# Performance work log

Measured on AMD Instinct MI355X. Metric: run time of the kernel, lower is better.

Reference implementation:

```python
import jax, jax.numpy as jnp
import numpy as np

B, S, CTX, DIM = 2, 2048, 2048, 2048
H, HKV, HD = 16, 4, 128
HID = 5464  # 4*ceil(int(4*DIM*2/3)/4)
EPS = 1.1920929e-07  # torch eps=None -> finfo(fp32).eps
REP = H // HKV


def rmsnorm(x, w):
    return x * jax.lax.rsqrt(jnp.mean(x * x, axis=-1, keepdims=True) + EPS) * w


def rotate_half(x):
    # interleaved rotate: out[::2] = -x[1::2], out[1::2] = x[::2]
    x2 = x.reshape(x.shape[:-1] + (-1, 2))
    return jnp.stack([-x2[..., 1], x2[..., 0]], axis=-1).reshape(x.shape)


def masked_attn(q, k, v, mask):
    # q,k,v: [B,H,Sq/Sk,D]; mask broadcastable to [B,H,Sq,Sk]
    scale = 1.0 / jnp.sqrt(jnp.asarray(q.shape[-1], q.dtype))
    s = jnp.einsum('bhqd,bhkd->bhqk', q, k) * scale
    s = jnp.where(mask, s, jnp.asarray(-1e30, s.dtype))
    p = jax.nn.softmax(s, axis=-1)
    p = jnp.where(mask, p, 0.0)  # fully-masked rows -> 0 output (flex_attention semantics)
    return jnp.einsum('bhqk,bhkd->bhqd', p, v)


def setup_inputs() -> dict:
    key = jax.random.key(0)
    ks = jax.random.split(key, 20)
    std = 0.02
    return {
        'x': jax.random.normal(ks[0], (B, S, DIM), jnp.float32),
        'context': jax.random.normal(ks[1], (B, CTX, DIM), jnp.float32),
        'freqs_cos': jax.random.uniform(ks[2], (S, 1, HD), jnp.float32),
        'freqs_sin': jax.random.uniform(ks[3], (S, 1, HD), jnp.float32),
        'wqkv': jax.random.normal(ks[4], ((H + 2 * HKV) * HD, DIM), jnp.float32) * std,
        'wo_self': jax.random.normal(ks[5], (DIM, DIM), jnp.float32) * std,
        'qn_self': jnp.ones((HD,), jnp.float32),
        'kn_self': jnp.ones((HD,), jnp.float32),
        'wq': jax.random.normal(ks[6], (H * HD, DIM), jnp.float32) * std,
        'wkv': jax.random.normal(ks[7], (2 * HKV * HD, DIM), jnp.float32) * std,
        'wo_cross': jax.random.normal(ks[8], (DIM, DIM), jnp.float32) * std,
        'qn_cross': jnp.ones((HD,), jnp.float32),
        'kn_cross': jnp.ones((HD,), jnp.float32),
        'w1': jax.random.normal(ks[9], (HID, DIM), jnp.float32) * std,
        'w2': jax.random.normal(ks[10], (DIM, HID), jnp.float32) * std,
        'attn_norm_w': jnp.ones((DIM,), jnp.float32),
        'cross_norm_w': jnp.ones((DIM,), jnp.float32),
        'ffn_norm_w': jnp.ones((DIM,), jnp.float32),
        'vis_mask': jax.random.randint(ks[11], (B, S), 0, 2).astype(bool),
        'context_mask': jax.random.randint(ks[12], (B, CTX), 0, 2).astype(bool),
    }


def reference(x, context, freqs_cos, freqs_sin, wqkv, wo_self, qn_self, kn_self,
              wq, wkv, wo_cross, qn_cross, kn_cross, w1, w2,
              attn_norm_w, cross_norm_w, ffn_norm_w, vis_mask, context_mask):
    b, s, _ = x.shape
    ctx = context.shape[1]

    # ---- self-attention (prenorm) ----
    h0 = rmsnorm(x, attn_norm_w)
    qkv = h0 @ wqkv.T
    xq = qkv[..., :H * HD].reshape(b, s, H, HD)
    xk = qkv[..., H * HD:(H + HKV) * HD].reshape(b, s, HKV, HD)
    xv = qkv[..., (H + HKV) * HD:].reshape(b, s, HKV, HD)
    xq = rmsnorm(xq, qn_self)   # qk-norm BEFORE rope in self-attn
    xk = rmsnorm(xk, kn_self)
    xq = xq * freqs_cos + rotate_half(xq) * freqs_sin
    xk = xk * freqs_cos + rotate_half(xk) * freqs_sin
    q = xq.transpose(0, 2, 1, 3)
    k = jnp.repeat(xk.transpose(0, 2, 1, 3), REP, axis=1)
    v = jnp.repeat(xv.transpose(0, 2, 1, 3), REP, axis=1)
    m_self = vis_mask[:, None, :, None] & vis_mask[:, None, None, :]
    a = masked_attn(q, k, v, m_self)
    h = x + a.transpose(0, 2, 1, 3).reshape(b, s, DIM) @ wo_self.T

    # ---- cross-attention (prenorm) ----
    hc = rmsnorm(h, cross_norm_w)
    xq = (hc @ wq.T).reshape(b, s, H, HD)
    kv = context @ wkv.T
    xk = kv[..., :HKV * HD].reshape(b, ctx, HKV, HD)
    xv = kv[..., HKV * HD:].reshape(b, ctx, HKV, HD)
    xq = xq * freqs_cos + rotate_half(xq) * freqs_sin  # rope on q BEFORE qk-norm in cross-attn
    xq = rmsnorm(xq, qn_cross)
    xk = rmsnorm(xk, kn_cross)
    q = xq.transpose(0, 2, 1, 3)
    k = jnp.repeat(xk.transpose(0, 2, 1, 3), REP, axis=1)
    v = jnp.repeat(xv.transpose(0, 2, 1, 3), REP, axis=1)
    m_cross = context_mask[:, None, None, :]
    a = masked_attn(q, k, v, m_cross)
    h = h + a.transpose(0, 2, 1, 3).reshape(b, s, DIM) @ wo_cross.T

    # ---- FFN (silu) ----
    hf = rmsnorm(h, ffn_norm_w)
    return h + jax.nn.silu(hf @ w1.T) @ w2.T
```

## Files before the change

### kernel.cpp

```cpp
#include <hip/hip_runtime.h>

#define DEVI __device__ __forceinline__

typedef __attribute__((ext_vector_type(4))) float f32x4;
typedef __attribute__((ext_vector_type(8))) __bf16 bf16x8;

static constexpr float EPS = 1.1920929e-07f;
static constexpr float SC2L = 0.12751551960234575f;

DEVI float bf2f(unsigned short u){ return __uint_as_float(((unsigned)u)<<16); }
DEVI unsigned short f2bfu(float f){
  unsigned u = __float_as_uint(f);
  u += 0x7fffu + ((u>>16)&1u);
  return (unsigned short)(u>>16);
}
DEVI unsigned pack2(float a, float b){ return (unsigned)f2bfu(a) | ((unsigned)f2bfu(b)<<16); }
DEVI float exp2a(float x){ float r; asm("v_exp_f32 %0, %1" : "=v"(r) : "v"(x)); return r; }
DEVI unsigned cvtpk(float lo, float hi){
  unsigned r; asm("v_cvt_pk_bf16_f32 %0, %1, %2" : "=v"(r) : "v"(lo), "v"(hi)); return r;
}

DEVI void gload16(const void* g, const void* l){
  __builtin_amdgcn_global_load_lds((const __attribute__((address_space(1))) void*)g,
                                   (__attribute__((address_space(3))) void*)l, 16, 0, 0);
}

__global__ void k_masknorm(const unsigned* __restrict__ vin, const unsigned* __restrict__ cin,
                           unsigned char* __restrict__ vout, unsigned char* __restrict__ cout){
  __shared__ int smode;
  const int t = threadIdx.x;
  if (t==0) smode = 0;
  __syncthreads();
  unsigned loc = 0;
  for (int i=t; i<1024; i+=256) loc |= (vin[i] > 1u);
  if (loc) smode = 1;
  __syncthreads();
  if (smode){
    for (int i=t; i<1024; i+=256){
      ((unsigned*)vout)[i] = vin[i];
      ((unsigned*)cout)[i] = cin[i];
    }
  } else {
    const int* vi = (const int*)vin; const int* ci = (const int*)cin;
    for (int i=t; i<4096; i+=256){
      vout[i] = (unsigned char)(vi[i] != 0);
      cout[i] = (unsigned char)(ci[i] != 0);
    }
  }
}

__global__ void k_conv(const float* __restrict__ s, unsigned short* __restrict__ d, int n4){
  int i = blockIdx.x*256 + threadIdx.x;
  if (i >= n4) return;
  float4 v = ((const float4*)s)[i];
  uint2 u; u.x = pack2(v.x, v.y); u.y = pack2(v.z, v.w);
  ((uint2*)d)[i] = u;
}
__global__ void k_convpad_rows(const float* __restrict__ s, unsigned short* __restrict__ d,
                               int R, int C, int Rp){
  int i = blockIdx.x*256 + threadIdx.x;
  int total = (Rp*C)>>2;
  if (i >= total) return;
  uint2 u; u.x = 0u; u.y = 0u;
  if (i*4 < R*C){ float4 v = ((const float4*)s)[i]; u.x = pack2(v.x,v.y); u.y = pack2(v.z,v.w); }
  ((uint2*)d)[i] = u;
}
__global__ void k_convpad_cols(const float* __restrict__ s, unsigned short* __restrict__ d,
                               int N, int K, int Kp){
  int i = blockIdx.x*256 + threadIdx.x;
  int total = (N*Kp)>>2;
  if (i >= total) return;
  int i4 = i*4; int n = i4/Kp; int k = i4 - n*Kp;
  uint2 u; u.x = 0u; u.y = 0u;
  if (k < K){ float4 v = *(const float4*)(s + (size_t)n*K + k); u.x = pack2(v.x,v.y); u.y = pack2(v.z,v.w); }
  ((uint2*)d)[i] = u;
}

__global__ void k_rms(const float* __restrict__ X, const float* __restrict__ W,
                      unsigned short* __restrict__ Y){
  const int row = blockIdx.x, tid = threadIdx.x;
  const float* x = X + (size_t)row*2048;
  float4 v0 = ((const float4*)x)[tid*2];
  float4 v1 = ((const float4*)x)[tid*2+1];
  float ss = v0.x*v0.x+v0.y*v0.y+v0.z*v0.z+v0.w*v0.w
           + v1.x*v1.x+v1.y*v1.y+v1.z*v1.z+v1.w*v1.w;
  #pragma unroll
  for (int o=32;o;o>>=1) ss += __shfl_xor(ss, o);
  __shared__ float red[4];
  if ((tid&63)==0) red[tid>>6] = ss;
  __syncthreads();
  float tot = red[0]+red[1]+red[2]+red[3];
  float rs = rsqrtf(tot*(1.0f/2048.0f) + EPS);
  float4 w0 = ((const float4*)W)[tid*2];
  float4 w1 = ((const float4*)W)[tid*2+1];
  uint4 u;
  u.x = pack2(v0.x*rs*w0.x, v0.y*rs*w0.y);
  u.y = pack2(v0.z*rs*w0.z, v0.w*rs*w0.w);
  u.z = pack2(v1.x*rs*w1.x, v1.y*rs*w1.y);
  u.w = pack2(v1.z*rs*w1.z, v1.w*rs*w1.w);
  *(uint4*)(Y + (size_t)row*2048 + tid*8) = u;
}

template<int EPI>
__global__ void k_gemm(const unsigned short* __restrict__ A, const unsigned short* __restrict__ Bw,
                       void* Cout, const float* resid, int M, int N, int K){
  __shared__ __align__(16) unsigned short sm[16384];
  const int tid = threadIdx.x;
  const int w = tid>>6, l = tid&63, g = l>>4, q = l&15;
  const int bm = blockIdx.y<<7, bn = blockIdx.x<<7;
  const int wr = (w>>1)<<6, wc = (w&1)<<6;
  f32x4 acc[4][4];
  #pragma unroll
  for (int a=0;a<4;++a)
    #pragma unroll
    for (int b2=0;b2<4;++b2) acc[a][b2] = f32x4{0.f,0.f,0.f,0.f};

  const unsigned short* Ag = A + (size_t)bm*K;
  const unsigned short* Bg = Bw + (size_t)bn*K;
  const int nk = K>>5;
  int cur = 0;

  auto STAGE = [&](int buf, int kt){
    #pragma unroll
    for (int i=0;i<2;++i){
      int L = (i*256+tid)*16;
      int r = L>>6; int ce = (L&63)>>1;
      int lofs = __builtin_amdgcn_readfirstlane(buf*8192 + i*4096 + (tid>>6)*1024);
      gload16(Ag + (size_t)r*K + (kt<<5) + ce, (const char*)sm + lofs);
    }
    #pragma unroll
    for (int i=0;i<2;++i){
      int L = (i*256+tid)*16;
      int r = L>>6; int ce = (L&63)>>1;
      int lofs = __builtin_amdgcn_readfirstlane(16384 + buf*8192 + i*4096 + (tid>>6)*1024);
      gload16(Bg + (size_t)r*K + (kt<<5) + ce, (const char*)sm + lofs);
    }
  };

  STAGE(0, 0);
  __syncthreads();
  for (int kt=0; kt<nk; ++kt){
    if (kt+1 < nk) STAGE(cur^1, kt+1);
    const unsigned short* Ab = sm + cur*4096;
    const unsigned short* Bb = sm + 8192 + cur*4096;
    bf16x8 af[4], bfr[4];
    #pragma unroll
    for (int mi=0;mi<4;++mi) af[mi] = *(const bf16x8*)(Ab + (wr + mi*16 + q)*32 + g*8);
    #pragma unroll
    for (int ni=0;ni<4;++ni) bfr[ni] = *(const bf16x8*)(Bb + (wc + ni*16 + q)*32 + g*8);
    #pragma unroll
    for (int mi=0;mi<4;++mi)
      #pragma unroll
      for (int ni=0;ni<4;++ni)
        acc[mi][ni] = __builtin_amdgcn_mfma_f32_16x16x32_bf16(af[mi], bfr[ni], acc[mi][ni], 0,0,0);
    __syncthreads();
    cur ^= 1;
  }
  #pragma unroll
  for (int mi=0;mi<4;++mi)
    #pragma unroll
    for (int ni=0;ni<4;++ni)
      #pragma unroll
      for (int r=0;r<4;++r){
        int row = bm + wr + mi*16 + g*4 + r;
        int col = bn + wc + ni*16 + q;
        size_t idx = (size_t)row*N + col;
        float v = acc[mi][ni][r];
        if (EPI==0) ((unsigned short*)Cout)[idx] = f2bfu(v);
        else if (EPI==1){ float sg = v/(1.0f+__expf(-v)); ((unsigned short*)Cout)[idx] = f2bfu(sg); }
        else ((float*)Cout)[idx] = resid[idx] + v;
      }
}

template<int EPI>
__global__ __launch_bounds__(512,1)
void k_gemm2(const unsigned short* __restrict__ A, const unsigned short* __restrict__ Bw,
             void* Cout, const float* resid, int M, int N, int K){
  __shared__ __align__(16) char sm[147456];
  const int tid = threadIdx.x;
  const int wid = tid>>6, l = tid&63, g = l>>4, q = l&15;
  const int wm = wid>>2, wn = wid&3;
  const int gy = gridDim.y;
  const int orig = blockIdx.y*gridDim.x + blockIdx.x;
  const int qq = (gridDim.x*gy)>>3;
  const int nid = (orig&7)*qq + (orig>>3);
  const int bm = (nid % gy) << 7;
  const int bn = (nid / gy) << 8;
  f32x4 acc[4][4];
  #pragma unroll
  for (int a=0;a<4;++a)
    #pragma unroll
    for (int b2=0;b2<4;++b2) acc[a][b2] = f32x4{0.f,0.f,0.f,0.f};

  const unsigned short* Ag = A + (size_t)bm*K;
  const unsigned short* Bg = Bw + (size_t)bn*K;
  const int nk = K>>6;

  auto STAGE_A = [&](int buf, int kt){
    #pragma unroll
    for (int j=0;j<2;++j){
      int L = (j*512+tid)*16;
      int lr = L>>7, c8 = (L>>4)&7;
      int cg = c8 ^ (lr&7);
      int lofs = __builtin_amdgcn_readfirstlane(buf*49152 + j*8192 + wid*1024);
      gload16(Ag + (size_t)lr*K + (kt<<6) + cg*8, sm + lofs);
    }
  };
  auto STAGE_B1 = [&](int buf, int kt, int j){
    int L = (j*512+tid)*16;
    int rn = L>>7, c8 = (L>>4)&7;
    int cg = c8 ^ (rn&7);
    int lofs = __builtin_amdgcn_readfirstlane(buf*49152 + 16384 + j*8192 + wid*1024);
    gload16(Bg + (size_t)rn*K + (kt<<6) + cg*8, sm + lofs);
  };

  STAGE_A(0,0); STAGE_B1(0,0,0); STAGE_B1(0,0,1); STAGE_B1(0,0,2); STAGE_B1(0,0,3);
  STAGE_A(1,1); STAGE_B1(1,1,0); STAGE_B1(1,1,1); STAGE_B1(1,1,2); STAGE_B1(1,1,3);

  int buf = 0;
  for (int kt=0; kt<nk; ++kt){
    int p2 = buf+2; if (p2>2) p2-=3;
    if (kt+1 < nk) asm volatile("s_waitcnt vmcnt(6)" ::: "memory");
    else           asm volatile("s_waitcnt vmcnt(0)" ::: "memory");
    asm volatile("s_waitcnt lgkmcnt(0)" ::: "memory");
    __builtin_amdgcn_s_barrier();
    asm volatile("" ::: "memory");

    const char* Ab = sm + buf*49152;
    const char* Bb = sm + buf*49152 + 16384;

    #pragma unroll
    for (int ks=0; ks<2; ++ks){
      if (kt+2 < nk){
        if (ks==0){ STAGE_A(p2, kt+2); STAGE_B1(p2, kt+2, 0); }
        else      { STAGE_B1(p2, kt+2, 1); STAGE_B1(p2, kt+2, 2); STAGE_B1(p2, kt+2, 3); }
      }
      bf16x8 af[4], bfr[4];
      #pragma unroll
      for (int mi=0;mi<4;++mi){
        int lr = wm*64 + mi*16 + q;
        af[mi] = *(const bf16x8*)(Ab + lr*128 + (((ks*4+g) ^ (lr&7))<<4));
      }
      #pragma unroll
      for (int ni=0;ni<4;++ni){
        int rn = wn*64 + ni*16 + q;
        bfr[ni] = *(const bf16x8*)(Bb + rn*128 + (((ks*4+g) ^ (rn&7))<<4));
      }
      asm volatile("s_waitcnt lgkmcnt(0)" ::: "memory");
      __builtin_amdgcn_s_setprio(1);
      #pragma unroll
      for (int mi=0;mi<4;++mi)
        #pragma unroll
        for (int ni=0;ni<4;++ni)
          acc[mi][ni] = __builtin_amdgcn_mfma_f32_16x16x32_bf16(af[mi], bfr[ni], acc[mi][ni], 0,0,0);
      __builtin_amdgcn_s_setprio(0);
    }
    buf = (buf==2) ? 0 : buf+1;
  }

  #pragma unroll
  for (int mi=0;mi<4;++mi)
    #pragma unroll
    for (int ni=0;ni<4;++ni)
      #pragma unroll
      for (int r=0;r<4;++r){
        int row = bm + wm*64 + mi*16 + g*4 + r;
        int col = bn + wn*64 + ni*16 + q;
        size_t idx = (size_t)row*N + col;
        float v = acc[mi][ni][r];
        if (EPI==0) ((unsigned short*)Cout)[idx] = f2bfu(v);
        else if (EPI==1){ float sg = v/(1.0f+__expf(-v)); ((unsigned short*)Cout)[idx] = f2bfu(sg); }
        else ((float*)Cout)[idx] = resid[idx] + v;
      }
}

__global__ void k_self_pp(const unsigned short* __restrict__ qkv, const float* __restrict__ fc,
                          const float* __restrict__ fs, const float* __restrict__ qn,
                          const float* __restrict__ kn,
                          unsigned short* __restrict__ Qb, unsigned short* __restrict__ Kb,
                          unsigned short* __restrict__ Vt){
  const int row = blockIdx.x;
  const int b = row>>11, s = row&2047;
  const int w = threadIdx.x>>6, l = threadIdx.x&63;
  const int d0 = 2*l, d1 = d0+1;
  const float c0 = fc[s*128+d0], c1 = fc[s*128+d1];
  const float s0 = fs[s*128+d0], s1 = fs[s*128+d1];
  #pragma unroll
  for (int it=0; it<6; ++it){
    const int hh = it*4 + w;
    const unsigned short* src = qkv + (size_t)row*3072 + hh*128;
    if (hh >= 20){
      const int hv = hh - 20;
      size_t base = ((size_t)(b*4 + hv))*128*2048;
      Vt[base + (size_t)d0*2048 + s] = src[d0];
      Vt[base + (size_t)d1*2048 + s] = src[d1];
    } else {
      float x0 = bf2f(src[d0]), x1 = bf2f(src[d1]);
      float ss = x0*x0 + x1*x1;
      #pragma unroll
      for (int o=32;o;o>>=1) ss += __shfl_xor(ss, o);
      float rs = rsqrtf(ss*(1.0f/128.0f) + EPS);
      if (hh < 16){
        float y0 = x0*rs*qn[d0], y1 = x1*rs*qn[d1];
        *(unsigned*)(Qb + (((size_t)(b*16 + hh)*2048 + s)*128) + d0)
          = pack2((y0*c0 - y1*s0)*SC2L, (y1*c1 + y0*s1)*SC2L);
      } else {
        float y0 = x0*rs*kn[d0], y1 = x1*rs*kn[d1];
        *(unsigned*)(Kb + (((size_t)(b*4 + (hh-16))*2048 + s)*128) + d0)
          = pack2(y0*c0 - y1*s0, y1*c1 + y0*s1);
      }
    }
  }
}

__global__ void k_crossq_pp(const unsigned short* __restrict__ qc, const float* __restrict__ fc,
                            const float* __restrict__ fs, const float* __restrict__ qn,
                            unsigned short* __restrict__ Qb){
  const int row = blockIdx.x;
  const int b = row>>11, s = row&2047;
  const int w = threadIdx.x>>6, l = threadIdx.x&63;
  const int d0 = 2*l, d1 = d0+1;
  const float c0 = fc[s*128+d0], c1 = fc[s*128+d1];
  const float s0 = fs[s*128+d0], s1 = fs[s*128+d1];
  #pragma unroll
  for (int it=0; it<4; ++it){
    const int hh = it*4 + w;
    const unsigned short* src = qc + (size_t)row*2048 + hh*128;
    float x0 = bf2f(src[d0]), x1 = bf2f(src[d1]);
    float y0 = x0*c0 - x1*s0;
    float y1 = x1*c1 + x0*s1;
    float ss = y0*y0 + y1*y1;
    #pragma unroll
    for (int o=32;o;o>>=1) ss += __shfl_xor(ss, o);
    float rs = rsqrtf(ss*(1.0f/128.0f) + EPS);
    *(unsigned*)(Qb + (((size_t)(b*16 + hh)*2048 + s)*128) + d0)
      = pack2(y0*rs*qn[d0]*SC2L, y1*rs*qn[d1]*SC2L);
  }
}

__global__ void k_crosskv_pp(const unsigned short* __restrict__ kvc, const float* __restrict__ kn,
                             unsigned short* __restrict__ Kb, unsigned short* __restrict__ Vt){
  const int row = blockIdx.x;
  const int b = row>>11, s = row&2047;
  const int w = threadIdx.x>>6, l = threadIdx.x&63;
  const int d0 = 2*l, d1 = d0+1;
  #pragma unroll
  for (int it=0; it<2; ++it){
    const int hh = it*4 + w;
    const unsigned short* src = kvc + (size_t)row*1024 + hh*128;
    if (hh < 4){
      float x0 = bf2f(src[d0]), x1 = bf2f(src[d1]);
      float ss = x0*x0 + x1*x1;
      #pragma unroll
      for (int o=32;o;o>>=1) ss += __shfl_xor(ss, o);
      float rs = rsqrtf(ss*(1.0f/128.0f) + EPS);
      *(unsigned*)(Kb + (((size_t)(b*4 + hh)*2048 + s)*128) + d0)
        = pack2(x0*rs*kn[d0], x1*rs*kn[d1]);
    } else {
      const int hv = hh-4;
      size_t base = ((size_t)(b*4 + hv))*128*2048;
      Vt[base + (size_t)d0*2048 + s] = src[d0];
      Vt[base + (size_t)d1*2048 + s] = src[d1];
    }
  }
}

template<bool QMASK>
__global__ __launch_bounds__(1024,1)
void k_attn(const unsigned short* __restrict__ Qg, const unsigned short* __restrict__ Kg,
            const unsigned short* __restrict__ Vtg,
            const unsigned char* __restrict__ qm, const unsigned char* __restrict__ km,
            unsigned short* __restrict__ Og, int H, int HKV){
  constexpr int SK = 2048, SQ = 2048, NT = SK/64;
  __shared__ __align__(16) char smem[106496];
  const int qt = blockIdx.x, hk = blockIdx.y, b = blockIdx.z;
  const int REP = H/HKV;
  const int tid = threadIdx.x, w = tid>>6, l = tid&63, g = l>>4, q = l&15;
  const int hq = w>>2, wsub = w&3;

  if (tid < 256){
    const unsigned long long mv = ((const unsigned long long*)(km + (size_t)b*SK))[tid];
    float* bl = (float*)(smem + 98304);
    #pragma unroll
    for (int j=0;j<8;++j)
      bl[tid*8+j] = ((mv>>(8*j)) & 0xffull) ? 0.0f : -3.0e38f;
  }

  const int h = hk*REP + hq;
  const size_t qrow = (size_t)(b*H + h)*SQ + qt*64 + wsub*16 + q;
  bf16x8 qf[4];
  #pragma unroll
  for (int ks=0;ks<4;++ks) qf[ks] = *(const bf16x8*)(Qg + qrow*128 + ks*32 + g*8);

  f32x4 oacc[8];
  #pragma unroll
  for (int i=0;i<8;++i) oacc[i] = f32x4{0.f,0.f,0.f,0.f};
  float m_run = -1.0e30f, l_run = 0.f;

  const unsigned short* Kt0 = Kg + (size_t)(b*HKV + hk)*SK*128;
  const unsigned short* Vt0 = Vtg + (size_t)(b*HKV + hk)*128*SK;
  const float* biasf = (const float*)(smem + 98304);
  char* Pl = smem + 65536 + w*2048;

  auto STAGE_T = [&](int t, int p){
    {
      int r = tid>>4, c16 = tid&15;
      int c = (c16 & 8) | ((c16 & 7) ^ (r & 7));
      int lofs = __builtin_amdgcn_readfirstlane(p*16384 + w*1024);
      gload16(Kt0 + (size_t)(t*64 + r)*128 + c*8, smem + lofs);
    }
    {
      int d = tid>>3, c8 = tid&7;
      int c = c8 ^ (d & 7);
      int lofs = __builtin_amdgcn_readfirstlane(32768 + p*16384 + w*1024);
      gload16(Vt0 + (size_t)d*SK + t*64 + c*8, smem + lofs);
    }
  };

  STAGE_T(0, 0);

  for (int t=0; t<NT; ++t){
    const int p = t&1;
    asm volatile("s_waitcnt lgkmcnt(0)" ::: "memory");
    __builtin_amdgcn_s_barrier();
    asm volatile("" ::: "memory");
    if (t+1 < NT){
      STAGE_T(t+1, p^1);
      asm volatile("s_waitcnt vmcnt(2)" ::: "memory");
    } else {
      asm volatile("s_waitcnt vmcnt(0)" ::: "memory");
    }
    __builtin_amdgcn_s_barrier();
    asm volatile("" ::: "memory");

    const char* Kb_ = smem + p*16384;
    const char* Vb_ = smem + 32768 + p*16384;

    f32x4 sacc[4];
    #pragma unroll
    for (int i=0;i<4;++i) sacc[i] = f32x4{0.f,0.f,0.f,0.f};
    __builtin_amdgcn_s_setprio(1);
    #pragma unroll
    for (int ks=0;ks<4;++ks){
      #pragma unroll
      for (int mi=0;mi<4;++mi){
        int kcol = mi*16 + q;
        int c = 4*ks + g;
        int c16 = (c & 8) | ((c & 7) ^ (kcol & 7));
        bf16x8 ak = *(const bf16x8*)(Kb_ + kcol*256 + c16*16);
        sacc[mi] = __builtin_amdgcn_mfma_f32_16x16x32_bf16(ak, qf[ks], sacc[mi], 0,0,0);
      }
    }
    __builtin_amdgcn_s_setprio(0);

    float sv[4][4];
    float mloc = -3.0e38f;
    #pragma unroll
    for (int mi=0;mi<4;++mi){
      f32x4 bb = *(const f32x4*)(biasf + t*64 + mi*16 + g*4);
      #pragma unroll
      for (int r=0;r<4;++r){
        float v = sacc[mi][r] + bb[r];
        sv[mi][r] = v;
        mloc = fmaxf(mloc, v);
      }
    }
    mloc = fmaxf(mloc, __shfl_xor(mloc, 16));
    mloc = fmaxf(mloc, __shfl_xor(mloc, 32));
    if (!__all(mloc - m_run <= 8.0f)){
      float mnew = fmaxf(m_run, mloc);
      float alpha = exp2a(m_run - mnew);
      l_run *= alpha;
      #pragma unroll
      for (int i=0;i<8;++i) oacc[i] *= alpha;
      m_run = mnew;
    }
    float rsum = 0.f;
    unsigned pb[4][2];
    #pragma unroll
    for (int mi=0;mi<4;++mi){
      float p0 = exp2a(sv[mi][0] - m_run);
      float p1 = exp2a(sv[mi][1] - m_run);
      float p2 = exp2a(sv[mi][2] - m_run);
      float p3 = exp2a(sv[mi][3] - m_run);
      rsum += (p0+p1)+(p2+p3);
      pb[mi][0] = cvtpk(p0, p1);
      pb[mi][1] = cvtpk(p2, p3);
    }
    rsum += __shfl_xor(rsum, 16);
    rsum += __shfl_xor(rsum, 32);
    l_run += rsum;

    #pragma unroll
    for (int mi=0;mi<4;++mi){
      int c16 = (2*mi + (g>>1)) ^ (q & 7);
      uint2 uu; uu.x = pb[mi][0]; uu.y = pb[mi][1];
      *(uint2*)(Pl + q*128 + c16*16 + (g&1)*8) = uu;
    }
    asm volatile("" ::: "memory");

    __builtin_amdgcn_s_setprio(1);
    #pragma unroll
    for (int ks=0;ks<2;++ks){
      int c16 = (4*ks + g) ^ (q & 7);
      bf16x8 pf = *(const bf16x8*)(Pl + q*128 + c16*16);
      #pragma unroll
      for (int mi=0;mi<8;++mi){
        int d = mi*16 + q;
        bf16x8 vf = *(const bf16x8*)(Vb_ + d*128 + c16*16);
        oacc[mi] = __builtin_amdgcn_mfma_f32_16x16x32_bf16(vf, pf, oacc[mi], 0,0,0);
      }
    }
    __builtin_amdgcn_s_setprio(0);
  }

  float inv = (l_run > 0.f) ? 1.0f/l_run : 0.f;
  if (QMASK){
    if (!qm[(size_t)b*SQ + qt*64 + wsub*16 + q]) inv = 0.f;
  }
  float* Ot = (float*)smem;
  const int qloc = tid>>4, seg = tid&15;
  #pragma unroll
  for (int ph=0; ph<4; ++ph){
    __syncthreads();
    if (hq == ph){
      #pragma unroll
      for (int mi=0;mi<8;++mi)
        #pragma unroll
        for (int r=0;r<4;++r){
          int d = mi*16 + g*4 + r;
          Ot[d*65 + wsub*16 + q] = oacc[mi][r]*inv;
        }
    }
    __syncthreads();
    int srow = qt*64 + qloc;
    size_t obase = ((size_t)b*SQ + srow)*(size_t)(H*128) + (size_t)(hk*REP + ph)*128 + seg*8;
    float vv[8];
    #pragma unroll
    for (int j=0;j<8;++j) vv[j] = Ot[(seg*8 + j)*65 + qloc];
    uint4 u;
    u.x = pack2(vv[0],vv[1]); u.y = pack2(vv[2],vv[3]);
    u.z = pack2(vv[4],vv[5]); u.w = pack2(vv[6],vv[7]);
    *(uint4*)(Og + obase) = u;
  }
}

extern "C" void kernel_launch(void* const* d_in, const int* in_sizes, int n_in,
                              void* d_out, int out_size, void* d_ws, size_t ws_size,
                              hipStream_t stream){
  const float* x        = (const float*)d_in[0];
  const float* ctx      = (const float*)d_in[1];
  const float* fc       = (const float*)d_in[2];
  const float* fs       = (const float*)d_in[3];
  const float* wqkv     = (const float*)d_in[4];
  const float* wo_self  = (const float*)d_in[5];
  const float* qn_self  = (const float*)d_in[6];
  const float* kn_self  = (const float*)d_in[7];
  const float* wq       = (const float*)d_in[8];
  const float* wkv      = (const float*)d_in[9];
  const float* wo_cross = (const float*)d_in[10];
  const float* qn_cross = (const float*)d_in[11];
  const float* kn_cross = (const float*)d_in[12];
  const float* w1       = (const float*)d_in[13];
  const float* w2       = (const float*)d_in[14];
  const float* attn_nw  = (const float*)d_in[15];
  const float* cross_nw = (const float*)d_in[16];
  const float* ffn_nw   = (const float*)d_in[17];
  const unsigned* vis_raw   = (const unsigned*)d_in[18];
  const unsigned* cmask_raw = (const unsigned*)d_in[19];
  float* out = (float*)d_out;

  char* ws = (char*)d_ws;
  unsigned short* wslot = (unsigned short*)(ws);
  unsigned short* ctxbf = (unsigned short*)(ws +  23068672);
  unsigned short* nbuf  = (unsigned short*)(ws +  39845888);
  unsigned short* qkvb  = (unsigned short*)(ws +  56623104);
  unsigned short* Qb    = (unsigned short*)(ws +  81788928);
  unsigned short* Kb    = (unsigned short*)(ws +  98566144);
  unsigned short* Vtb   = (unsigned short*)(ws + 102760448);
  unsigned short* aob   = (unsigned short*)(ws + 106954752);
  unsigned short* midb  = (unsigned short*)(ws + 106954752);
  unsigned char*  visN  = (unsigned char*)(ws + 153092096);
  unsigned char*  cmkN  = (unsigned char*)(ws + 153096192);
  unsigned short* qcb   = qkvb;
  unsigned short* kvcb  = qkvb + 8388608;

  auto conv = [&](const float* s, unsigned short* dst, size_t n){
    int n4 = (int)(n>>2);
    k_conv<<<(n4+255)/256, 256, 0, stream>>>(s, dst, n4);
  };

  k_masknorm<<<1,256,0,stream>>>(vis_raw, cmask_raw, visN, cmkN);

  conv(ctx, ctxbf, (size_t)4096*2048);
  k_rms<<<4096,256,0,stream>>>(x, attn_nw, nbuf);
  conv(wqkv, wslot, (size_t)3072*2048);
  k_gemm2<0><<<dim3(12,32),512,0,stream>>>(nbuf, wslot, qkvb, nullptr, 4096,3072,2048);
  k_self_pp<<<4096,256,0,stream>>>(qkvb, fc, fs, qn_self, kn_self, Qb, Kb, Vtb);
  k_attn<true><<<dim3(32,4,2),1024,0,stream>>>(Qb, Kb, Vtb, visN, visN, aob, 16, 4);
  conv(wo_self, wslot, (size_t)2048*2048);
  k_gemm2<2><<<dim3(8,32),512,0,stream>>>(aob, wslot, out, x, 4096,2048,2048);

  k_rms<<<4096,256,0,stream>>>(out, cross_nw, nbuf);
  conv(wq, wslot, (size_t)2048*2048);
  k_gemm2<0><<<dim3(8,32),512,0,stream>>>(nbuf, wslot, qcb, nullptr, 4096,2048,2048);
  conv(wkv, wslot, (size_t)1024*2048);
  k_gemm<0><<<dim3(8,32),256,0,stream>>>(ctxbf, wslot, kvcb, nullptr, 4096,1024,2048);
  k_crossq_pp<<<4096,256,0,stream>>>(qcb, fc, fs, qn_cross, Qb);
  k_crosskv_pp<<<4096,256,0,stream>>>(kvcb, kn_cross, Kb, Vtb);
  k_attn<false><<<dim3(32,4,2),1024,0,stream>>>(Qb, Kb, Vtb, nullptr, cmkN, aob, 16, 4);
  conv(wo_cross, wslot, (size_t)2048*2048);
  k_gemm2<2><<<dim3(8,32),512,0,stream>>>(aob, wslot, out, out, 4096,2048,2048);

  k_rms<<<4096,256,0,stream>>>(out, ffn_nw, nbuf);
  k_convpad_rows<<<(5632*2048/4+255)/256,256,0,stream>>>(w1, wslot, 5464, 2048, 5632);
  k_gemm2<1><<<dim3(22,32),512,0,stream>>>(nbuf, wslot, midb, nullptr, 4096,5632,2048);
  k_convpad_cols<<<(2048*5632/4+255)/256,256,0,stream>>>(w2, wslot, 2048, 5464, 5632);
  k_gemm2<2><<<dim3(8,32),512,0,stream>>>(midb, wslot, out, out, 4096,2048,5632);

  (void)in_sizes; (void)n_in; (void)out_size; (void)ws_size;
}
```

Baseline: 765.2 us.

## Halve GEMM K-tile to 32 to cut LDS and allow multiple blocks per CU

Shrinks the k_gemm2 K step from 64 to 32, so the triple-buffered LDS footprint drops from 144KB to 72KB. The launch bound is raised to allow up to 4 blocks per CU, and the swizzle and staging are rewritten for 64-byte rows. Prefetch is now issued once per iteration ahead of the fragment loads, with a sched_barrier added. The goal is more resident waves to hide memory latency, at the cost of twice as many barriers and a shorter MFMA run per synchronization. A register cap from the new launch bound could cause spills.

```diff
diff --git a/kernel.cpp b/kernel.cpp
--- a/kernel.cpp
+++ b/kernel.cpp
@@ -173,10 +173,10 @@
 }
 
 template<int EPI>
-__global__ __launch_bounds__(512,1)
+__global__ __launch_bounds__(512,4)
 void k_gemm2(const unsigned short* __restrict__ A, const unsigned short* __restrict__ Bw,
              void* Cout, const float* resid, int M, int N, int K){
-  __shared__ __align__(16) char sm[147456];
+  __shared__ __align__(16) char sm[73728];
   const int tid = threadIdx.x;
   const int wid = tid>>6, l = tid&63, g = l>>4, q = l&15;
   const int wm = wid>>2, wn = wid&3;
@@ -194,67 +194,59 @@
 
   const unsigned short* Ag = A + (size_t)bm*K;
   const unsigned short* Bg = Bw + (size_t)bn*K;
-  const int nk = K>>6;
+  const int nk = K>>5;
 
   auto STAGE_A = [&](int buf, int kt){
+    int lr = tid>>2, c8 = tid&3;
+    int cg = c8 ^ ((lr>>1)&3);
+    int lofs = __builtin_amdgcn_readfirstlane(buf*24576 + wid*1024);
+    gload16(Ag + (size_t)lr*K + (kt<<5) + cg*8, sm + lofs);
+  };
+  auto STAGE_B = [&](int buf, int kt){
     #pragma unroll
     for (int j=0;j<2;++j){
-      int L = (j*512+tid)*16;
-      int lr = L>>7, c8 = (L>>4)&7;
-      int cg = c8 ^ (lr&7);
-      int lofs = __builtin_amdgcn_readfirstlane(buf*49152 + j*8192 + wid*1024);
-      gload16(Ag + (size_t)lr*K + (kt<<6) + cg*8, sm + lofs);
+      int rn = (j*512+tid)>>2, c8 = tid&3;
+      int cg = c8 ^ ((rn>>1)&3);
+      int lofs = __builtin_amdgcn_readfirstlane(buf*24576 + 8192 + j*8192 + wid*1024);
+      gload16(Bg + (size_t)rn*K + (kt<<5) + cg*8, sm + lofs);
     }
   };
-  auto STAGE_B1 = [&](int buf, int kt, int j){
-    int L = (j*512+tid)*16;
-    int rn = L>>7, c8 = (L>>4)&7;
-    int cg = c8 ^ (rn&7);
-    int lofs = __builtin_amdgcn_readfirstlane(buf*49152 + 16384 + j*8192 + wid*1024);
-    gload16(Bg + (size_t)rn*K + (kt<<6) + cg*8, sm + lofs);
-  };
-
-  STAGE_A(0,0); STAGE_B1(0,0,0); STAGE_B1(0,0,1); STAGE_B1(0,0,2); STAGE_B1(0,0,3);
-  STAGE_A(1,1); STAGE_B1(1,1,0); STAGE_B1(1,1,1); STAGE_B1(1,1,2); STAGE_B1(1,1,3);
+
+  STAGE_A(0,0); STAGE_B(0,0);
+  STAGE_A(1,1); STAGE_B(1,1);
 
   int buf = 0;
   for (int kt=0; kt<nk; ++kt){
     int p2 = buf+2; if (p2>2) p2-=3;
-    if (kt+1 < nk) asm volatile("s_waitcnt vmcnt(6)" ::: "memory");
+    if (kt+1 < nk) asm volatile("s_waitcnt vmcnt(3)" ::: "memory");
     else           asm volatile("s_waitcnt vmcnt(0)" ::: "memory");
     asm volatile("s_waitcnt lgkmcnt(0)" ::: "memory");
     __builtin_amdgcn_s_barrier();
     asm volatile("" ::: "memory");
-
-    const char* Ab = sm + buf*49152;
-    const char* Bb = sm + buf*49152 + 16384;
-
-    #pragma unroll
-    for (int ks=0; ks<2; ++ks){
-      if (kt+2 < nk){
-        if (ks==0){ STAGE_A(p2, kt+2); STAGE_B1(p2, kt+2, 0); }
-        else      { STAGE_B1(p2, kt+2, 1); STAGE_B1(p2, kt+2, 2); STAGE_B1(p2, kt+2, 3); }
-      }
-      bf16x8 af[4], bfr[4];
-      #pragma unroll
-      for (int mi=0;mi<4;++mi){
-        int lr = wm*64 + mi*16 + q;
-        af[mi] = *(const bf16x8*)(Ab + lr*128 + (((ks*4+g) ^ (lr&7))<<4));
-      }
-      #pragma unroll
-      for (int ni=0;ni<4;++ni){
-        int rn = wn*64 + ni*16 + q;
-        bfr[ni] = *(const bf16x8*)(Bb + rn*128 + (((ks*4+g) ^ (rn&7))<<4));
-      }
-      asm volatile("s_waitcnt lgkmcnt(0)" ::: "memory");
-      __builtin_amdgcn_s_setprio(1);
-      #pragma unroll
-      for (int mi=0;mi<4;++mi)
-        #pragma unroll
-        for (int ni=0;ni<4;++ni)
-          acc[mi][ni] = __builtin_amdgcn_mfma_f32_16x16x32_bf16(af[mi], bfr[ni], acc[mi][ni], 0,0,0);
-      __builtin_amdgcn_s_setprio(0);
-    }
+    if (kt+2 < nk){ STAGE_A(p2, kt+2); STAGE_B(p2, kt+2); }
+
+    const char* Ab = sm + buf*24576;
+    const char* Bb = Ab + 8192;
+    bf16x8 af[4], bfr[4];
+    #pragma unroll
+    for (int mi=0;mi<4;++mi){
+      int lr = wm*64 + mi*16 + q;
+      af[mi] = *(const bf16x8*)(Ab + lr*64 + ((g ^ ((lr>>1)&3))<<4));
+    }
+    #pragma unroll
+    for (int ni=0;ni<4;++ni){
+      int rn = wn*64 + ni*16 + q;
+      bfr[ni] = *(const bf16x8*)(Bb + rn*64 + ((g ^ ((rn>>1)&3))<<4));
+    }
+    asm volatile("s_waitcnt lgkmcnt(0)" ::: "memory");
+    __builtin_amdgcn_sched_barrier(0);
+    __builtin_amdgcn_s_setprio(1);
+    #pragma unroll
+    for (int mi=0;mi<4;++mi)
+      #pragma unroll
+      for (int ni=0;ni<4;++ni)
+        acc[mi][ni] = __builtin_amdgcn_mfma_f32_16x16x32_bf16(af[mi], bfr[ni], acc[mi][ni], 0,0,0);
+    __builtin_amdgcn_s_setprio(0);
     buf = (buf==2) ? 0 : buf+1;
   }
 
```

After: 796.9 us. +4.1%, slower.

## Shrink attention blocks to 512 threads and single-buffer K/V for higher occupancy

Applied to the files above, without the earlier changes.

The attention kernel now uses 512-thread blocks covering 32 query rows instead of 1024 threads over 64 rows. The grid doubles and launch bounds allow 4 blocks per CU. The K/V double buffer is dropped in favour of one staged buffer with a full vmcnt(0) wait, which cuts LDS enough that several blocks fit per CU. Latency hiding moves from software prefetch to running many blocks at once, at the cost of twice the K/V global traffic per query and a loss of load/compute overlap within each block.

```diff
diff --git a/kernel.cpp b/kernel.cpp
--- a/kernel.cpp
+++ b/kernel.cpp
@@ -366,28 +366,28 @@
 }
 
 template<bool QMASK>
-__global__ __launch_bounds__(1024,1)
+__global__ __launch_bounds__(512,4)
 void k_attn(const unsigned short* __restrict__ Qg, const unsigned short* __restrict__ Kg,
             const unsigned short* __restrict__ Vtg,
             const unsigned char* __restrict__ qm, const unsigned char* __restrict__ km,
             unsigned short* __restrict__ Og, int H, int HKV){
   constexpr int SK = 2048, SQ = 2048, NT = SK/64;
-  __shared__ __align__(16) char smem[106496];
+  __shared__ __align__(16) char smem[57344];
   const int qt = blockIdx.x, hk = blockIdx.y, b = blockIdx.z;
   const int REP = H/HKV;
   const int tid = threadIdx.x, w = tid>>6, l = tid&63, g = l>>4, q = l&15;
-  const int hq = w>>2, wsub = w&3;
+  const int hq = w>>1, wsub = w&1;
 
   if (tid < 256){
     const unsigned long long mv = ((const unsigned long long*)(km + (size_t)b*SK))[tid];
-    float* bl = (float*)(smem + 98304);
+    float* bl = (float*)(smem + 49152);
     #pragma unroll
     for (int j=0;j<8;++j)
       bl[tid*8+j] = ((mv>>(8*j)) & 0xffull) ? 0.0f : -3.0e38f;
   }
 
   const int h = hk*REP + hq;
-  const size_t qrow = (size_t)(b*H + h)*SQ + qt*64 + wsub*16 + q;
+  const size_t qrow = (size_t)(b*H + h)*SQ + qt*32 + wsub*16 + q;
   bf16x8 qf[4];
   #pragma unroll
   for (int ks=0;ks<4;++ks) qf[ks] = *(const bf16x8*)(Qg + qrow*128 + ks*32 + g*8);
@@ -399,42 +399,39 @@
 
   const unsigned short* Kt0 = Kg + (size_t)(b*HKV + hk)*SK*128;
   const unsigned short* Vt0 = Vtg + (size_t)(b*HKV + hk)*128*SK;
-  const float* biasf = (const float*)(smem + 98304);
-  char* Pl = smem + 65536 + w*2048;
-
-  auto STAGE_T = [&](int t, int p){
-    {
-      int r = tid>>4, c16 = tid&15;
+  const float* biasf = (const float*)(smem + 49152);
+  char* Pl = smem + 32768 + w*2048;
+
+  auto STAGE_T = [&](int t){
+    #pragma unroll
+    for (int j=0;j<2;++j){
+      int idx = j*512 + tid;
+      int r = idx>>4, c16 = idx&15;
       int c = (c16 & 8) | ((c16 & 7) ^ (r & 7));
-      int lofs = __builtin_amdgcn_readfirstlane(p*16384 + w*1024);
+      int lofs = __builtin_amdgcn_readfirstlane(j*8192 + w*1024);
       gload16(Kt0 + (size_t)(t*64 + r)*128 + c*8, smem + lofs);
     }
-    {
-      int d = tid>>3, c8 = tid&7;
+    #pragma unroll
+    for (int j=0;j<2;++j){
+      int idx = j*512 + tid;
+      int d = idx>>3, c8 = idx&7;
       int c = c8 ^ (d & 7);
-      int lofs = __builtin_amdgcn_readfirstlane(32768 + p*16384 + w*1024);
+      int lofs = __builtin_amdgcn_readfirstlane(16384 + j*8192 + w*1024);
       gload16(Vt0 + (size_t)d*SK + t*64 + c*8, smem + lofs);
     }
   };
 
-  STAGE_T(0, 0);
-
   for (int t=0; t<NT; ++t){
-    const int p = t&1;
     asm volatile("s_waitcnt lgkmcnt(0)" ::: "memory");
     __builtin_amdgcn_s_barrier();
     asm volatile("" ::: "memory");
-    if (t+1 < NT){
-      STAGE_T(t+1, p^1);
-      asm volatile("s_waitcnt vmcnt(2)" ::: "memory");
-    } else {
-      asm volatile("s_waitcnt vmcnt(0)" ::: "memory");
-    }
+    STAGE_T(t);
+    asm volatile("s_waitcnt vmcnt(0)" ::: "memory");
     __builtin_amdgcn_s_barrier();
     asm volatile("" ::: "memory");
 
-    const char* Kb_ = smem + p*16384;
-    const char* Vb_ = smem + 32768 + p*16384;
+    const char* Kb_ = smem;
+    const char* Vb_ = smem + 16384;
 
     f32x4 sacc[4];
     #pragma unroll
@@ -516,7 +513,7 @@
 
   float inv = (l_run > 0.f) ? 1.0f/l_run : 0.f;
   if (QMASK){
-    if (!qm[(size_t)b*SQ + qt*64 + wsub*16 + q]) inv = 0.f;
+    if (!qm[(size_t)b*SQ + qt*32 + wsub*16 + q]) inv = 0.f;
   }
   float* Ot = (float*)smem;
   const int qloc = tid>>4, seg = tid&15;
@@ -529,15 +526,15 @@
         #pragma unroll
         for (int r=0;r<4;++r){
           int d = mi*16 + g*4 + r;
-          Ot[d*65 + wsub*16 + q] = oacc[mi][r]*inv;
+          Ot[d*33 + wsub*16 + q] = oacc[mi][r]*inv;
         }
     }
     __syncthreads();
-    int srow = qt*64 + qloc;
+    int srow = qt*32 + qloc;
     size_t obase = ((size_t)b*SQ + srow)*(size_t)(H*128) + (size_t)(hk*REP + ph)*128 + seg*8;
     float vv[8];
     #pragma unroll
-    for (int j=0;j<8;++j) vv[j] = Ot[(seg*8 + j)*65 + qloc];
+    for (int j=0;j<8;++j) vv[j] = Ot[(seg*8 + j)*33 + qloc];
     uint4 u;
     u.x = pack2(vv[0],vv[1]); u.y = pack2(vv[2],vv[3]);
     u.z = pack2(vv[4],vv[5]); u.w = pack2(vv[6],vv[7]);
@@ -597,7 +594,7 @@
   conv(wqkv, wslot, (size_t)3072*2048);
   k_gemm2<0><<<dim3(12,32),512,0,stream>>>(nbuf, wslot, qkvb, nullptr, 4096,3072,2048);
   k_self_pp<<<4096,256,0,stream>>>(qkvb, fc, fs, qn_self, kn_self, Qb, Kb, Vtb);
-  k_attn<true><<<dim3(32,4,2),1024,0,stream>>>(Qb, Kb, Vtb, visN, visN, aob, 16, 4);
+  k_attn<true><<<dim3(64,4,2),512,0,stream>>>(Qb, Kb, Vtb, visN, visN, aob, 16, 4);
   conv(wo_self, wslot, (size_t)2048*2048);
   k_gemm2<2><<<dim3(8,32),512,0,stream>>>(aob, wslot, out, x, 4096,2048,2048);
 
@@ -608,7 +605,7 @@
   k_gemm<0><<<dim3(8,32),256,0,stream>>>(ctxbf, wslot, kvcb, nullptr, 4096,1024,2048);
   k_crossq_pp<<<4096,256,0,stream>>>(qcb, fc, fs, qn_cross, Qb);
   k_crosskv_pp<<<4096,256,0,stream>>>(kvcb, kn_cross, Kb, Vtb);
-  k_attn<false><<<dim3(32,4,2),1024,0,stream>>>(Qb, Kb, Vtb, nullptr, cmkN, aob, 16, 4);
+  k_attn<false><<<dim3(64,4,2),512,0,stream>>>(Qb, Kb, Vtb, nullptr, cmkN, aob, 16, 4);
   conv(wo_cross, wslot, (size_t)2048*2048);
   k_gemm2<2><<<dim3(8,32),512,0,stream>>>(aob, wslot, out, out, 4096,2048,2048);
 
```

Result: no change. 771.5 us (+0.8%).
